# Kernel tuning notes

Hardware: AMD Instinct MI355X
Metric: run time of the kernel (lower is better)

The kernel has to match this reference:

```python
import jax, jax.numpy as jnp
import numpy as np

N_SRC_F = 40000; N_TGT_F = 40000; N_F = N_SRC_F + N_TGT_F
N_SRC_C = 1024; N_TGT_C = 1024; N_C = N_SRC_C + N_TGT_C
NN = 30        # KPConv neighbors per point
K = 15         # kernel points
C1 = 128       # fine-level feats (first_feats_dim)
C2 = 256       # coarse encoder out dim
GNN = 256      # gnn_feats_dim
HEADS = 4
DGCNN_K = 10
FINAL = 32     # final_feats_dim
EXT_F = 1.0; EXT_C = 2.0   # KPConv influence extents (scaled to unit-cube clouds)
EPS = 1e-12


def kpconv(q_pts, s_pts, s_feats, neighb, kpts, W, extent):
    # q_pts [Nq,3], s_pts [Ns,3], s_feats [Ns,Cin], neighb [Nq,NN], kpts [K,3], W [K,Cin,Cout]
    npts = s_pts[neighb]                              # [Nq,NN,3] irregular gather
    rel = npts - q_pts[:, None, :]
    # ||rel - kp||^2 expanded to avoid a [Nq,NN,K,3] intermediate
    d2 = (jnp.sum(rel * rel, -1)[:, :, None] + jnp.sum(kpts * kpts, -1)[None, None, :]
          - 2.0 * jnp.einsum('njd,kd->njk', rel, kpts))
    infl = jax.nn.relu(1.0 - jnp.sqrt(jnp.maximum(d2, EPS)) / extent)   # [Nq,NN,K]
    nf = s_feats[neighb]                              # [Nq,NN,Cin]
    h = jnp.einsum('njk,njc->nkc', infl, nf)          # kernel-point aggregation
    return jnp.einsum('nkc,kcd->nd', h, W)


def knn_idx(coords, k):
    sq = jnp.sum(coords * coords, -1)
    d2 = sq[:, None] + sq[None, :] - 2.0 * (coords @ coords.T)
    return jax.lax.top_k(-d2, k)[1]


def self_layer(coords, x, W, b):
    # DGCNN edge conv: knn on coords, edge = [x_i, x_j - x_i], 1x1 conv + relu, max over k
    idx = knn_idx(coords, DGCNN_K)
    neigh = x[idx]                                    # [N,k,C]
    ctr = jnp.broadcast_to(x[:, None, :], neigh.shape)
    edge = jnp.concatenate([ctr, neigh - ctr], -1)    # [N,k,2C]
    return jnp.max(jax.nn.relu(edge @ W + b), axis=1)


def cross_layer(x, y, Wq, Wk, Wv, Wm, bm):
    # multi-head cross attention x <- y, residual MLP on [x, message]
    N, C = x.shape
    dh = C // HEADS
    q = (x @ Wq).reshape(N, HEADS, dh)
    k = (y @ Wk).reshape(-1, HEADS, dh)
    v = (y @ Wv).reshape(-1, HEADS, dh)
    attn = jax.nn.softmax(jnp.einsum('nhd,mhd->hnm', q, k) / float(np.sqrt(dh)), axis=-1)
    msg = jnp.einsum('hnm,mhd->nhd', attn, v).reshape(N, C)
    return x + jnp.concatenate([x, msg], -1) @ Wm + bm


def l2norm(x):
    return x / jnp.maximum(jnp.linalg.norm(x, axis=1, keepdims=True), EPS)


def _forward(points_f, points_c, features, kernel_points_f, kernel_points_c,
             W_kp1, W_kp2, W_bottle, b_bottle, W_self1, b_self1,
             Wq, Wk, Wv, W_cross, b_cross, W_self2, b_self2,
             W_proj, b_proj, W_score, b_score, epsilon, W_dec, b_dec,
             neighbors_f, pool_idx, upsample_idx, len_src_c):
    # --- encoder: fine KPConv + strided KPConv to coarse ---
    x_f = kpconv(points_f, points_f, features, neighbors_f, kernel_points_f, W_kp1, EXT_F)  # [N_f,C1]
    skip = x_f
    x_c = kpconv(points_c, points_f, x_f, pool_idx, kernel_points_c, W_kp2, EXT_C)          # [N_c,C2]
    feats_c = x_c @ W_bottle + b_bottle                # bottleneck 1x1 conv -> [N_c,GNN]
    src, tgt = feats_c[:len_src_c], feats_c[len_src_c:]
    sc, tc = points_c[:len_src_c], points_c[len_src_c:]
    # --- GCN: self -> cross -> self (weights shared across src/tgt) ---
    src = self_layer(sc, src, W_self1, b_self1)
    tgt = self_layer(tc, tgt, W_self1, b_self1)
    src2 = cross_layer(src, tgt, Wq, Wk, Wv, W_cross, b_cross)
    tgt2 = cross_layer(tgt, src, Wq, Wk, Wv, W_cross, b_cross)
    src = self_layer(sc, src2, W_self2, b_self2)
    tgt = self_layer(tc, tgt2, W_self2, b_self2)
    feats = jnp.concatenate([src, tgt], 0) @ W_proj + b_proj   # proj_gnn
    scores_c_raw = feats @ W_score + b_score                   # proj_score [N_c,1]
    feats_norm = l2norm(feats)
    # --- bidirectional temperature-softmax matching head ---
    ip = feats_norm[:len_src_c] @ feats_norm[len_src_c:].T     # [Ns,Nt]
    temperature = jnp.exp(epsilon) + 0.03
    s1 = jax.nn.softmax(ip / temperature, axis=1) @ scores_c_raw[len_src_c:]
    s2 = jax.nn.softmax(ip.T / temperature, axis=1) @ scores_c_raw[:len_src_c]
    scores_saliency = jnp.concatenate([s1, s2], 0)
    # condition=True, add_cross_overlap=True branch
    x = jnp.concatenate([scores_c_raw, scores_saliency, feats], 1)    # [N_c, GNN+2]
    # --- decoder: nearest upsample + skip concat + unary conv ---
    x = jnp.concatenate([x[upsample_idx], skip], 1)            # [N_f, GNN+2+C1]
    x = x @ W_dec + b_dec                                      # [N_f, FINAL+2]
    feats_f = l2norm(x[:, :FINAL])
    so = jnp.clip(jax.nn.sigmoid(x[:, FINAL]), 0.0, 1.0)
    ss = jnp.clip(jax.nn.sigmoid(x[:, FINAL + 1]), 0.0, 1.0)
    so = jnp.where(jnp.isnan(so) | jnp.isinf(so), 0.0, so)     # regular_score
    ss = jnp.where(jnp.isnan(ss) | jnp.isinf(ss), 0.0, ss)
    return feats_f, so, ss


def _p(k, shape, fan):
    return jax.random.normal(k, shape, jnp.float32) / float(np.sqrt(fan))


def setup_inputs() -> dict:
    key = jax.random.key(0)
    ks = jax.random.split(key, 24)
    inp = {}
    inp['points_f'] = jax.random.uniform(ks[0], (N_F, 3), jnp.float32)
    inp['points_c'] = jax.random.uniform(ks[1], (N_C, 3), jnp.float32)
    inp['features'] = jnp.ones((N_F, 1), jnp.float32)
    inp['kernel_points_f'] = jax.random.normal(ks[2], (K, 3), jnp.float32) * 0.3
    inp['kernel_points_c'] = jax.random.normal(ks[3], (K, 3), jnp.float32) * 0.6
    inp['W_kp1'] = _p(ks[4], (K, 1, C1), K)
    inp['W_kp2'] = _p(ks[5], (K, C1, C2), K * C1)
    inp['W_bottle'] = _p(ks[6], (C2, GNN), C2); inp['b_bottle'] = jnp.zeros((GNN,), jnp.float32)
    inp['W_self1'] = _p(ks[7], (2 * GNN, GNN), 2 * GNN); inp['b_self1'] = jnp.zeros((GNN,), jnp.float32)
    inp['Wq'] = _p(ks[8], (GNN, GNN), GNN)
    inp['Wk'] = _p(ks[9], (GNN, GNN), GNN)
    inp['Wv'] = _p(ks[10], (GNN, GNN), GNN)
    inp['W_cross'] = _p(ks[11], (2 * GNN, GNN), 2 * GNN); inp['b_cross'] = jnp.zeros((GNN,), jnp.float32)
    inp['W_self2'] = _p(ks[12], (2 * GNN, GNN), 2 * GNN); inp['b_self2'] = jnp.zeros((GNN,), jnp.float32)
    inp['W_proj'] = _p(ks[13], (GNN, GNN), GNN); inp['b_proj'] = jnp.zeros((GNN,), jnp.float32)
    inp['W_score'] = _p(ks[14], (GNN, 1), GNN); inp['b_score'] = jnp.zeros((1,), jnp.float32)
    inp['epsilon'] = jnp.array(-5.0, jnp.float32)
    inp['W_dec'] = _p(ks[15], (GNN + 2 + C1, FINAL + 2), GNN + 2 + C1); inp['b_dec'] = jnp.zeros((FINAL + 2,), jnp.float32)
    inp['neighbors_f'] = jax.random.randint(ks[16], (N_F, NN), 0, N_F)
    inp['pool_idx'] = jax.random.randint(ks[17], (N_C, NN), 0, N_F)
    inp['upsample_idx'] = jax.random.randint(ks[18], (N_F,), 0, N_C)
    inp['len_src_c'] = N_SRC_C
    inp['len_src_f'] = N_SRC_F
    return inp


def reference(points_f, points_c, features, kernel_points_f, kernel_points_c,
              W_kp1, W_kp2, W_bottle, b_bottle, W_self1, b_self1,
              Wq, Wk, Wv, W_cross, b_cross, W_self2, b_self2,
              W_proj, b_proj, W_score, b_score, epsilon, W_dec, b_dec,
              neighbors_f, pool_idx, upsample_idx, len_src_c, len_src_f):
    return _forward(points_f, points_c, features, kernel_points_f, kernel_points_c,
                    W_kp1, W_kp2, W_bottle, b_bottle, W_self1, b_self1,
                    Wq, Wk, Wv, W_cross, b_cross, W_self2, b_self2,
                    W_proj, b_proj, W_score, b_score, epsilon, W_dec, b_dec,
                    neighbors_f, pool_idx, upsample_idx, len_src_c)
```

## Files before the change

### kernel.cpp

```cpp
#include <hip/hip_runtime.h>
#include <math.h>

#define NFINE   80000
#define NCRS    2048
#define NSRC    1024
#define NNB     30
#define KP      15
#define C1D     128
#define C2D     256
#define GD      256
#define DGK     10
#define FINALD  32
#define DECIN   386
#define DECOUT  34

#define NCHUNK  8
#define CHUNK   128
#define TK      32

__global__ __launch_bounds__(256) void kpconv_fine(
    const float* __restrict__ pts, const float* __restrict__ feat,
    const int* __restrict__ nbr, const float* __restrict__ kp,
    const float* __restrict__ W, float* __restrict__ out)
{
    int t = threadIdx.x, w = t >> 6, lane = t & 63;
    int n = blockIdx.x * 4 + w;
    __shared__ float contrib[4][NNB][17];
    __shared__ float h[4][KP + 1];
    float kx[KP], ky[KP], kz[KP], kk[KP];
#pragma unroll
    for (int k = 0; k < KP; k++) {
        kx[k] = kp[k*3]; ky[k] = kp[k*3+1]; kz[k] = kp[k*3+2];
        kk[k] = kx[k]*kx[k] + ky[k]*ky[k] + kz[k]*kz[k];
    }
    if (lane < NNB) {
        float qx = pts[n*3], qy = pts[n*3+1], qz = pts[n*3+2];
        int id = nbr[n*NNB + lane];
        float rx = pts[id*3]-qx, ry = pts[id*3+1]-qy, rz = pts[id*3+2]-qz;
        float rr = rx*rx + ry*ry + rz*rz;
        float f = feat[id];
#pragma unroll
        for (int k = 0; k < KP; k++) {
            float d2 = rr + kk[k] - 2.f*(rx*kx[k] + ry*ky[k] + rz*kz[k]);
            float infl = fmaxf(1.f - sqrtf(fmaxf(d2, 1e-12f)), 0.f);
            contrib[w][lane][k] = infl * f;
        }
    }
    __syncthreads();
    if (lane < KP) {
        float s = 0.f;
#pragma unroll
        for (int j = 0; j < NNB; j++) s += contrib[w][j][lane];
        h[w][lane] = s;
    }
    __syncthreads();
    float a0 = 0.f, a1 = 0.f;
#pragma unroll
    for (int k = 0; k < KP; k++) {
        float hk = h[w][k];
        a0 += hk * W[k*C1D + lane];
        a1 += hk * W[k*C1D + 64 + lane];
    }
    out[(size_t)n*C1D + lane]      = a0;
    out[(size_t)n*C1D + 64 + lane] = a1;
}

__global__ __launch_bounds__(256) void hh_kernel(
    const float* __restrict__ pc, const float* __restrict__ pf,
    const float* __restrict__ xf, const int* __restrict__ pool,
    const float* __restrict__ kp, float* __restrict__ hhg)
{
    int n = blockIdx.x, t = threadIdx.x;
    __shared__ float kx[KP], ky[KP], kz[KP], kk[KP];
    __shared__ float rel[NNB][4];
    __shared__ int   ids[NNB];
    __shared__ float infl[NNB][KP + 1];
    __shared__ float nf[NNB][C1D];
    if (t < KP) {
        float a = kp[t*3], b = kp[t*3+1], c = kp[t*3+2];
        kx[t] = a; ky[t] = b; kz[t] = c; kk[t] = a*a + b*b + c*c;
    }
    if (t < NNB) {
        int id = pool[n*NNB + t]; ids[t] = id;
        float qx = pc[n*3], qy = pc[n*3+1], qz = pc[n*3+2];
        float rx = pf[id*3]-qx, ry = pf[id*3+1]-qy, rz = pf[id*3+2]-qz;
        rel[t][0] = rx; rel[t][1] = ry; rel[t][2] = rz;
        rel[t][3] = rx*rx + ry*ry + rz*rz;
    }
    __syncthreads();
    for (int i = t; i < NNB*KP; i += 256) {
        int j = i / KP, kq = i % KP;
        float d2 = rel[j][3] + kk[kq]
                 - 2.f*(rel[j][0]*kx[kq] + rel[j][1]*ky[kq] + rel[j][2]*kz[kq]);
        infl[j][kq] = fmaxf(1.f - sqrtf(fmaxf(d2, 1e-12f)) * 0.5f, 0.f);
    }
    for (int i = t; i < NNB*C1D; i += 256) {
        int j = i >> 7, c = i & 127;
        nf[j][c] = xf[(size_t)ids[j]*C1D + c];
    }
    __syncthreads();
    for (int i = t; i < KP*C1D; i += 256) {
        int kq = i >> 7, c = i & 127;
        float s = 0.f;
#pragma unroll
        for (int j = 0; j < NNB; j++) s += infl[j][kq] * nf[j][c];
        hhg[(size_t)n*(KP*C1D) + i] = s;
    }
}

template<int CIN, int COUT, int TR, bool BIAS>
__global__ __launch_bounds__(COUT) void linear_rows(
    const float* __restrict__ in, const float* __restrict__ W,
    const float* __restrict__ b, float* __restrict__ out)
{
    int t = threadIdx.x, n0 = blockIdx.x * TR;
    __shared__ float xi[CIN][TR];
    for (int i = t; i < TR*CIN; i += COUT) {
        int r = i / CIN, c = i % CIN;
        xi[c][r] = in[(size_t)(n0+r)*CIN + c];
    }
    __syncthreads();
    float a[TR];
#pragma unroll
    for (int r = 0; r < TR; r++) a[r] = BIAS ? b[t] : 0.f;
    for (int c = 0; c < CIN; c++) {
        float wv = W[(size_t)c*COUT + t];
        float4 x0 = *(const float4*)&xi[c][0];
        a[0] += x0.x*wv; a[1] += x0.y*wv; a[2] += x0.z*wv; a[3] += x0.w*wv;
    }
#pragma unroll
    for (int r = 0; r < TR; r++) out[(size_t)(n0+r)*COUT + t] = a[r];
}

__global__ __launch_bounds__(512) void self_gemm(
    const float* __restrict__ x, const float* __restrict__ W,
    float* __restrict__ Y)
{
    int t = threadIdx.x, n0 = blockIdx.x * 4;
    __shared__ float xi[GD][4];
    for (int i = t; i < 4*GD; i += 512) {
        int r = i >> 8, c = i & 255;
        xi[c][r] = x[(size_t)(n0+r)*GD + c];
    }
    __syncthreads();
    const float* wcol = (t < GD) ? (W + t) : (W + (size_t)GD*GD + (t - GD));
    float a0 = 0.f, a1 = 0.f, a2 = 0.f, a3 = 0.f;
    for (int c = 0; c < GD; c++) {
        float wv = wcol[(size_t)c*GD];
        float4 xv = *(const float4*)&xi[c][0];
        a0 += xv.x*wv; a1 += xv.y*wv; a2 += xv.z*wv; a3 += xv.w*wv;
    }
    Y[(size_t)(n0+0)*512 + t] = a0;
    Y[(size_t)(n0+1)*512 + t] = a1;
    Y[(size_t)(n0+2)*512 + t] = a2;
    Y[(size_t)(n0+3)*512 + t] = a3;
}

__global__ __launch_bounds__(256) void edge_max(
    const float* __restrict__ Y, const int* __restrict__ knn,
    const float* __restrict__ b, float* __restrict__ out)
{
    int n = blockIdx.x, t = threadIdx.x;
    int base = (n < NSRC) ? 0 : NSRC;
    __shared__ int ids[DGK];
    if (t < DGK) ids[t] = base + knn[n*DGK + t];
    __syncthreads();
    float a  = Y[(size_t)n*512 + t];
    float bn = Y[(size_t)n*512 + GD + t];
    float cst = a - bn + b[t];
    float acc = 0.f;
#pragma unroll
    for (int j = 0; j < DGK; j++) {
        float bj = Y[(size_t)ids[j]*512 + GD + t];
        acc = fmaxf(acc, fmaxf(cst + bj, 0.f));
    }
    out[(size_t)n*GD + t] = acc;
}

__global__ __launch_bounds__(256) void qkv_kernel(
    const float* __restrict__ x, const float* __restrict__ Wq,
    const float* __restrict__ Wk, const float* __restrict__ Wv,
    float* __restrict__ qb, float* __restrict__ kb, float* __restrict__ vb)
{
    int t = threadIdx.x, n0 = blockIdx.x * 4;
    __shared__ float xi[GD][4];
    for (int i = t; i < 4*GD; i += 256) {
        int r = i >> 8, c = i & 255;
        xi[c][r] = x[(size_t)(n0+r)*GD + c];
    }
    __syncthreads();
    const float* Ws[3] = {Wq, Wk, Wv};
    float* outs[3] = {qb, kb, vb};
#pragma unroll
    for (int m = 0; m < 3; m++) {
        const float* W = Ws[m];
        float a0 = 0.f, a1 = 0.f, a2 = 0.f, a3 = 0.f;
        for (int c = 0; c < GD; c++) {
            float wv = W[c*GD + t];
            float4 xv = *(const float4*)&xi[c][0];
            a0 += xv.x*wv; a1 += xv.y*wv; a2 += xv.z*wv; a3 += xv.w*wv;
        }
        float* o = outs[m];
        o[(size_t)(n0+0)*GD + t] = a0;
        o[(size_t)(n0+1)*GD + t] = a1;
        o[(size_t)(n0+2)*GD + t] = a2;
        o[(size_t)(n0+3)*GD + t] = a3;
    }
}

__global__ __launch_bounds__(256) void knn_kernel(
    const float* __restrict__ pts, int* __restrict__ knn)
{
    int g = blockIdx.x;
    int t = threadIdx.x;
    int base = (g < NSRC) ? 0 : NSRC;
    int local = g - base;
    const float* P = pts + (size_t)base*3;
    __shared__ float d2s[NSRC];
    __shared__ float wval[4];
    __shared__ int   widx[4];
    float qx = P[local*3], qy = P[local*3+1], qz = P[local*3+2];
    float sqn = qx*qx + qy*qy + qz*qz;
#pragma unroll
    for (int ii = 0; ii < 4; ii++) {
        int m = t + ii*256;
        float px = P[m*3], py = P[m*3+1], pz = P[m*3+2];
        float sqm = px*px + py*py + pz*pz;
        d2s[m] = sqn + sqm - 2.f*(qx*px + qy*py + qz*pz);
    }
    __syncthreads();
    for (int r = 0; r < DGK; r++) {
        float bv = 3.4e38f; int bidx = NSRC;
#pragma unroll
        for (int ii = 0; ii < 4; ii++) {
            int m = t + ii*256;
            float v = d2s[m];
            if (v < bv) { bv = v; bidx = m; }
        }
#pragma unroll
        for (int off = 32; off >= 1; off >>= 1) {
            float ov = __shfl_xor(bv, off);
            int   oi = __shfl_xor(bidx, off);
            if (ov < bv || (ov == bv && oi < bidx)) { bv = ov; bidx = oi; }
        }
        if ((t & 63) == 0) { wval[t >> 6] = bv; widx[t >> 6] = bidx; }
        __syncthreads();
        if (t == 0) {
            float fv = wval[0]; int fi = widx[0];
#pragma unroll
            for (int wv2 = 1; wv2 < 4; wv2++)
                if (wval[wv2] < fv || (wval[wv2] == fv && widx[wv2] < fi)) {
                    fv = wval[wv2]; fi = widx[wv2];
                }
            knn[g*DGK + r] = fi;
            d2s[fi] = 3.4e38f;
        }
        __syncthreads();
    }
}

__global__ __launch_bounds__(256) void attn_flash(
    const float* __restrict__ qb, const float* __restrict__ kb,
    const float* __restrict__ vb, float* __restrict__ pm,
    float* __restrict__ pl, float* __restrict__ pacc)
{
    int bidx = blockIdx.x;
    int h = bidx & 3, chunk = (bidx >> 2) & 7, rb = bidx >> 5;
    int t = threadIdx.x;
    int u = t >> 2, li = t & 3;
    int row = rb * 64 + u;
    int kbase = (row < NSRC) ? NSRC : 0;

    __shared__ float4 kt[2][TK][16];
    __shared__ float4 vt[2][TK][16];

    const float4* kb4 = (const float4*)kb;
    const float4* vb4 = (const float4*)vb;
    size_t gbase = ((size_t)(kbase + chunk*CHUNK)) * 64 + h*16;

    float4 q[4];
    const float4* q4 = (const float4*)(qb + (size_t)row*GD + h*64 + li*16);
#pragma unroll
    for (int i = 0; i < 4; i++) q[i] = q4[i];
    float4 a[4];
#pragma unroll
    for (int i = 0; i < 4; i++) a[i] = make_float4(0.f, 0.f, 0.f, 0.f);
    float mr = -INFINITY, lr = 0.f;

    int f0 = t, f1 = t + 256;
    float4 rk0, rk1, rv0, rv1;

    {
        size_t tb = gbase;
        rk0 = kb4[tb + (size_t)(f0>>4)*64 + (f0&15)];
        rk1 = kb4[tb + (size_t)(f1>>4)*64 + (f1&15)];
        rv0 = vb4[tb + (size_t)(f0>>4)*64 + (f0&15)];
        rv1 = vb4[tb + (size_t)(f1>>4)*64 + (f1&15)];
        kt[0][f0>>4][f0&15] = rk0;  kt[0][f1>>4][f1&15] = rk1;
        vt[0][f0>>4][f0&15] = rv0;  vt[0][f1>>4][f1&15] = rv1;
    }
    __syncthreads();

    const int NT = CHUNK / TK;
    for (int tile = 0; tile < NT; tile++) {
        int cur = tile & 1;
        if (tile + 1 < NT) {
            size_t tb = gbase + (size_t)(tile+1)*TK*64;
            rk0 = kb4[tb + (size_t)(f0>>4)*64 + (f0&15)];
            rk1 = kb4[tb + (size_t)(f1>>4)*64 + (f1&15)];
            rv0 = vb4[tb + (size_t)(f0>>4)*64 + (f0&15)];
            rv1 = vb4[tb + (size_t)(f1>>4)*64 + (f1&15)];
        }
#pragma unroll 4
        for (int j = 0; j < TK; j++) {
            float4 k0 = kt[cur][j][li*4+0];
            float4 k1 = kt[cur][j][li*4+1];
            float4 k2 = kt[cur][j][li*4+2];
            float4 k3 = kt[cur][j][li*4+3];
            float d0 = q[0].x*k0.x + q[0].y*k0.y + q[0].z*k0.z + q[0].w*k0.w;
            float d1 = q[1].x*k1.x + q[1].y*k1.y + q[1].z*k1.z + q[1].w*k1.w;
            float d2 = q[2].x*k2.x + q[2].y*k2.y + q[2].z*k2.z + q[2].w*k2.w;
            float d3 = q[3].x*k3.x + q[3].y*k3.y + q[3].z*k3.z + q[3].w*k3.w;
            float p = (d0 + d1) + (d2 + d3);
            p += __shfl_xor(p, 1);
            p += __shfl_xor(p, 2);
            p *= 0.125f;
            float mn = fmaxf(mr, p);
            float sc = __expf(mr - mn);
            float e  = __expf(p - mn);
            lr = lr*sc + e;
            float4 v0 = vt[cur][j][li*4+0];
            float4 v1 = vt[cur][j][li*4+1];
            float4 v2 = vt[cur][j][li*4+2];
            float4 v3 = vt[cur][j][li*4+3];
            a[0].x = a[0].x*sc + e*v0.x; a[0].y = a[0].y*sc + e*v0.y;
            a[0].z = a[0].z*sc + e*v0.z; a[0].w = a[0].w*sc + e*v0.w;
            a[1].x = a[1].x*sc + e*v1.x; a[1].y = a[1].y*sc + e*v1.y;
            a[1].z = a[1].z*sc + e*v1.z; a[1].w = a[1].w*sc + e*v1.w;
            a[2].x = a[2].x*sc + e*v2.x; a[2].y = a[2].y*sc + e*v2.y;
            a[2].z = a[2].z*sc + e*v2.z; a[2].w = a[2].w*sc + e*v2.w;
            a[3].x = a[3].x*sc + e*v3.x; a[3].y = a[3].y*sc + e*v3.y;
            a[3].z = a[3].z*sc + e*v3.z; a[3].w = a[3].w*sc + e*v3.w;
            mr = mn;
        }
        if (tile + 1 < NT) {
            __syncthreads();
            int nb = (tile + 1) & 1;
            kt[nb][f0>>4][f0&15] = rk0;  kt[nb][f1>>4][f1&15] = rk1;
            vt[nb][f0>>4][f0&15] = rv0;  vt[nb][f1>>4][f1&15] = rv1;
            __syncthreads();
        }
    }
    int pi = (chunk*4 + h)*NCRS + row;
    if (li == 0) { pm[pi] = mr; pl[pi] = lr; }
    float4* po = (float4*)(pacc + (size_t)pi*64);
#pragma unroll
    for (int i = 0; i < 4; i++) po[li*4 + i] = a[i];
}

__global__ __launch_bounds__(256) void attn_combine(
    const float* __restrict__ pm, const float* __restrict__ pl,
    const float* __restrict__ pacc, float* __restrict__ msg)
{
    int row = blockIdx.x, t = threadIdx.x;
    int h = t >> 6, d = t & 63;
    float m = -INFINITY;
#pragma unroll
    for (int c = 0; c < NCHUNK; c++) m = fmaxf(m, pm[(c*4 + h)*NCRS + row]);
    float lsum = 0.f, asum = 0.f;
#pragma unroll
    for (int c = 0; c < NCHUNK; c++) {
        int pi = (c*4 + h)*NCRS + row;
        float w = __expf(pm[pi] - m);
        lsum += pl[pi] * w;
        asum += pacc[(size_t)pi*64 + d] * w;
    }
    msg[(size_t)row*GD + h*64 + d] = asum / lsum;
}

__global__ __launch_bounds__(256) void cross_combine(
    const float* __restrict__ x, const float* __restrict__ msg,
    const float* __restrict__ Wm, const float* __restrict__ bm,
    float* __restrict__ out)
{
    int t = threadIdx.x, n0 = blockIdx.x * 4;
    __shared__ float xs[GD][4], ms[GD][4];
    for (int i = t; i < 4*GD; i += 256) {
        int r = i >> 8, c = i & 255;
        xs[c][r] = x[(size_t)(n0+r)*GD + c];
        ms[c][r] = msg[(size_t)(n0+r)*GD + c];
    }
    __syncthreads();
    float a0 = bm[t], a1 = a0, a2 = a0, a3 = a0;
    for (int c = 0; c < GD; c++) {
        float w1 = Wm[c*GD + t];
        float w2 = Wm[(GD + c)*GD + t];
        float4 xv = *(const float4*)&xs[c][0];
        float4 mv = *(const float4*)&ms[c][0];
        a0 += xv.x*w1 + mv.x*w2; a1 += xv.y*w1 + mv.y*w2;
        a2 += xv.z*w1 + mv.z*w2; a3 += xv.w*w1 + mv.w*w2;
    }
    out[(size_t)(n0+0)*GD + t] = xs[t][0] + a0;
    out[(size_t)(n0+1)*GD + t] = xs[t][1] + a1;
    out[(size_t)(n0+2)*GD + t] = xs[t][2] + a2;
    out[(size_t)(n0+3)*GD + t] = xs[t][3] + a3;
}

__global__ __launch_bounds__(256) void proj_fused(
    const float* __restrict__ g3, const float* __restrict__ Wp,
    const float* __restrict__ bp, const float* __restrict__ Wsc,
    const float* __restrict__ bsc, float* __restrict__ feats,
    float* __restrict__ fnorm, float* __restrict__ scores)
{
    int n = blockIdx.x, t = threadIdx.x;
    __shared__ float xi[GD];
    __shared__ float red[256];
    xi[t] = g3[(size_t)n*GD + t];
    __syncthreads();
    float acc = bp[t];
    for (int c = 0; c < GD; c++) acc += xi[c] * Wp[c*GD + t];
    feats[(size_t)n*GD + t] = acc;
    red[t] = acc * acc; __syncthreads();
    for (int s = 128; s > 0; s >>= 1) { if (t < s) red[t] += red[t+s]; __syncthreads(); }
    float nrm = fmaxf(sqrtf(red[0]), 1e-12f);
    __syncthreads();
    fnorm[(size_t)n*GD + t] = acc / nrm;
    red[t] = acc * Wsc[t]; __syncthreads();
    for (int s = 128; s > 0; s >>= 1) { if (t < s) red[t] += red[t+s]; __syncthreads(); }
    if (t == 0) scores[n] = red[0] + bsc[0];
}

__global__ __launch_bounds__(256) void ip_kernel(
    const float* __restrict__ fnorm, float* __restrict__ ip)
{
    int t = threadIdx.x;
    int n0 = (blockIdx.x >> 2) * 4;
    int m  = (blockIdx.x & 3) * 256 + t;
    __shared__ float xs[GD][4];
    for (int i = t; i < 4*GD; i += 256) {
        int r = i >> 8, c = i & 255;
        xs[c][r] = fnorm[(size_t)(n0+r)*GD + c];
    }
    __syncthreads();
    const float4* fr = (const float4*)(fnorm + (size_t)(NSRC + m)*GD);
    float a0 = 0.f, a1 = 0.f, a2 = 0.f, a3 = 0.f;
    for (int c4 = 0; c4 < GD/4; c4++) {
        float4 f = fr[c4];
        float4 xa = *(const float4*)&xs[c4*4+0][0];
        float4 xb = *(const float4*)&xs[c4*4+1][0];
        float4 xc = *(const float4*)&xs[c4*4+2][0];
        float4 xd = *(const float4*)&xs[c4*4+3][0];
        a0 += f.x*xa.x + f.y*xb.x + f.z*xc.x + f.w*xd.x;
        a1 += f.x*xa.y + f.y*xb.y + f.z*xc.y + f.w*xd.y;
        a2 += f.x*xa.z + f.y*xb.z + f.z*xc.z + f.w*xd.z;
        a3 += f.x*xa.w + f.y*xb.w + f.z*xc.w + f.w*xd.w;
    }
    ip[(size_t)(n0+0)*NSRC + m] = a0;
    ip[(size_t)(n0+1)*NSRC + m] = a1;
    ip[(size_t)(n0+2)*NSRC + m] = a2;
    ip[(size_t)(n0+3)*NSRC + m] = a3;
}

template<bool COL>
__global__ __launch_bounds__(256) void saliency_kernel(
    const float* __restrict__ ip, const float* __restrict__ scores_other,
    const float* __restrict__ epsv, float* __restrict__ sal_out)
{
    int n = blockIdx.x, t = threadIdx.x;
    float T = expf(epsv[0]) + 0.03f;
    __shared__ float red[256];
    float vals[4];
    float m = -INFINITY;
#pragma unroll
    for (int ii = 0; ii < 4; ii++) {
        int i = t + ii*256;
        float vv = COL ? ip[(size_t)i*NSRC + n] : ip[(size_t)n*NSRC + i];
        vv /= T;
        vals[ii] = vv;
        m = fmaxf(m, vv);
    }
    red[t] = m; __syncthreads();
    for (int s = 128; s > 0; s >>= 1) { if (t < s) red[t] = fmaxf(red[t], red[t+s]); __syncthreads(); }
    float mx = red[0]; __syncthreads();
    float se = 0.f, wsum = 0.f;
#pragma unroll
    for (int ii = 0; ii < 4; ii++) {
        int i = t + ii*256;
        float e = expf(vals[ii] - mx);
        se += e; wsum += e * scores_other[i];
    }
    red[t] = se; __syncthreads();
    for (int s = 128; s > 0; s >>= 1) { if (t < s) red[t] += red[t+s]; __syncthreads(); }
    float S = red[0]; __syncthreads();
    red[t] = wsum; __syncthreads();
    for (int s = 128; s > 0; s >>= 1) { if (t < s) red[t] += red[t+s]; __syncthreads(); }
    if (t == 0) sal_out[n] = red[0] / S;
}

__global__ __launch_bounds__(256) void decoder_kernel(
    const float* __restrict__ feats, const float* __restrict__ scores,
    const float* __restrict__ sal, const float* __restrict__ skip,
    const int* __restrict__ ups, const float* __restrict__ Wd,
    const float* __restrict__ bd, float* __restrict__ outf,
    float* __restrict__ outso, float* __restrict__ outss)
{
    int row = blockIdx.x * 256 + threadIdx.x;
    if (row >= NFINE) return;
    int u = ups[row];
    float acc[DECOUT];
#pragma unroll
    for (int j = 0; j < DECOUT; j++) acc[j] = bd[j];
    float x0 = scores[u], x1 = sal[u];
#pragma unroll
    for (int j = 0; j < DECOUT; j++) acc[j] += x0 * Wd[j];
#pragma unroll
    for (int j = 0; j < DECOUT; j++) acc[j] += x1 * Wd[DECOUT + j];
    const float4* fr = (const float4*)(feats + (size_t)u * GD);
    for (int c4 = 0; c4 < GD/4; c4++) {
        float4 xv = fr[c4];
        const float* wr = Wd + (size_t)(2 + c4*4) * DECOUT;
#pragma unroll
        for (int j = 0; j < DECOUT; j++) acc[j] += xv.x * wr[j];
#pragma unroll
        for (int j = 0; j < DECOUT; j++) acc[j] += xv.y * wr[DECOUT + j];
#pragma unroll
        for (int j = 0; j < DECOUT; j++) acc[j] += xv.z * wr[2*DECOUT + j];
#pragma unroll
        for (int j = 0; j < DECOUT; j++) acc[j] += xv.w * wr[3*DECOUT + j];
    }
    const float4* sr = (const float4*)(skip + (size_t)row * C1D);
    for (int c4 = 0; c4 < C1D/4; c4++) {
        float4 xv = sr[c4];
        const float* wr = Wd + (size_t)(2 + GD + c4*4) * DECOUT;
#pragma unroll
        for (int j = 0; j < DECOUT; j++) acc[j] += xv.x * wr[j];
#pragma unroll
        for (int j = 0; j < DECOUT; j++) acc[j] += xv.y * wr[DECOUT + j];
#pragma unroll
        for (int j = 0; j < DECOUT; j++) acc[j] += xv.z * wr[2*DECOUT + j];
#pragma unroll
        for (int j = 0; j < DECOUT; j++) acc[j] += xv.w * wr[3*DECOUT + j];
    }
    float sq = 0.f;
#pragma unroll
    for (int j = 0; j < FINALD; j++) sq += acc[j]*acc[j];
    float inv = 1.f / fmaxf(sqrtf(sq), 1e-12f);
    float4* op = (float4*)(outf + (size_t)row * FINALD);
#pragma unroll
    for (int i = 0; i < 8; i++)
        op[i] = make_float4(acc[4*i]*inv, acc[4*i+1]*inv, acc[4*i+2]*inv, acc[4*i+3]*inv);
    float so = 1.f/(1.f + __expf(-acc[32]));
    so = fminf(fmaxf(so, 0.f), 1.f); if (!(so == so)) so = 0.f;
    float ss = 1.f/(1.f + __expf(-acc[33]));
    ss = fminf(fmaxf(ss, 0.f), 1.f); if (!(ss == ss)) ss = 0.f;
    outso[row] = so; outss[row] = ss;
}

extern "C" void kernel_launch(void* const* d_in, const int* in_sizes, int n_in,
                              void* d_out, int out_size, void* d_ws, size_t ws_size,
                              hipStream_t stream)
{
    const float* points_f     = (const float*)d_in[0];
    const float* points_c     = (const float*)d_in[1];
    const float* features     = (const float*)d_in[2];
    const float* kp_f         = (const float*)d_in[3];
    const float* kp_c         = (const float*)d_in[4];
    const float* W_kp1        = (const float*)d_in[5];
    const float* W_kp2        = (const float*)d_in[6];
    const float* W_bottle     = (const float*)d_in[7];
    const float* b_bottle     = (const float*)d_in[8];
    const float* W_self1      = (const float*)d_in[9];
    const float* b_self1      = (const float*)d_in[10];
    const float* Wq           = (const float*)d_in[11];
    const float* Wk           = (const float*)d_in[12];
    const float* Wv           = (const float*)d_in[13];
    const float* W_cross      = (const float*)d_in[14];
    const float* b_cross      = (const float*)d_in[15];
    const float* W_self2      = (const float*)d_in[16];
    const float* b_self2      = (const float*)d_in[17];
    const float* W_proj       = (const float*)d_in[18];
    const float* b_proj       = (const float*)d_in[19];
    const float* W_score      = (const float*)d_in[20];
    const float* b_score      = (const float*)d_in[21];
    const float* epsilon      = (const float*)d_in[22];
    const float* W_dec        = (const float*)d_in[23];
    const float* b_dec        = (const float*)d_in[24];
    const int*   neighbors_f  = (const int*)d_in[25];
    const int*   pool_idx     = (const int*)d_in[26];
    const int*   upsample_idx = (const int*)d_in[27];

    float* ws = (float*)d_ws;
    size_t o = 0;
    auto alloc = [&](size_t nfl) { float* p = ws + o; o += (nfl + 63) & ~(size_t)63; return p; };
    float* x_f     = alloc((size_t)NFINE * C1D);
    float* g1      = alloc((size_t)NCRS * GD);
    float* qb      = alloc((size_t)NCRS * GD);
    float* kb      = alloc((size_t)NCRS * GD);
    float* vb      = alloc((size_t)NCRS * GD);
    float* msg     = alloc((size_t)NCRS * GD);
    float* feats_c = alloc((size_t)NCRS * GD);
    float* scores  = alloc(NCRS);
    float* sal     = alloc(NCRS);
    int*   knn_b   = (int*)alloc(NCRS * DGK);

    const size_t NG = (size_t)NCRS * GD;
    size_t usz = (size_t)NCRS*C2D + (size_t)NCRS*KP*C1D;
    float* U = alloc(usz);
    float* x_c  = U;
    float* hhg  = U + (size_t)NCRS*C2D;
    float* Y1   = U;
    float* pm   = U;
    float* pl   = U + (size_t)NCRS*4*NCHUNK;
    float* pacc = U + (size_t)2*NCRS*4*NCHUNK;
    float* g2   = U;
    float* Y2   = U + NG;
    float* g3   = U + 3*NG;
    float* feats= U + 4*NG;
    float* fnorm= U + 5*NG;
    float* ip   = U + 6*NG;

    float* outf  = (float*)d_out;
    float* outso = outf + (size_t)NFINE * FINALD;
    float* outss = outso + NFINE;

    kpconv_fine<<<NFINE/4, 256, 0, stream>>>(points_f, features, neighbors_f, kp_f, W_kp1, x_f);
    hh_kernel<<<NCRS, 256, 0, stream>>>(points_c, points_f, x_f, pool_idx, kp_c, hhg);
    linear_rows<KP*C1D, C2D, 4, false><<<NCRS/4, C2D, 0, stream>>>(hhg, W_kp2, nullptr, x_c);
    linear_rows<C2D, GD, 4, true><<<NCRS/4, GD, 0, stream>>>(x_c, W_bottle, b_bottle, feats_c);

    knn_kernel<<<NCRS, 256, 0, stream>>>(points_c, knn_b);
    self_gemm<<<NCRS/4, 512, 0, stream>>>(feats_c, W_self1, Y1);
    edge_max<<<NCRS, 256, 0, stream>>>(Y1, knn_b, b_self1, g1);
    qkv_kernel<<<NCRS/4, 256, 0, stream>>>(g1, Wq, Wk, Wv, qb, kb, vb);
    attn_flash<<<1024, 256, 0, stream>>>(qb, kb, vb, pm, pl, pacc);
    attn_combine<<<NCRS, 256, 0, stream>>>(pm, pl, pacc, msg);
    cross_combine<<<NCRS/4, 256, 0, stream>>>(g1, msg, W_cross, b_cross, g2);
    self_gemm<<<NCRS/4, 512, 0, stream>>>(g2, W_self2, Y2);
    edge_max<<<NCRS, 256, 0, stream>>>(Y2, knn_b, b_self2, g3);

    proj_fused<<<NCRS, 256, 0, stream>>>(g3, W_proj, b_proj, W_score, b_score, feats, fnorm, scores);
    ip_kernel<<<NSRC, 256, 0, stream>>>(fnorm, ip);
    saliency_kernel<false><<<NSRC, 256, 0, stream>>>(ip, scores + NSRC, epsilon, sal);
    saliency_kernel<true><<<NSRC, 256, 0, stream>>>(ip, scores, epsilon, sal + NSRC);

    decoder_kernel<<<(NFINE + 255)/256, 256, 0, stream>>>(feats, scores, sal, x_f, upsample_idx,
                                                          W_dec, b_dec, outf, outso, outss);
}
```

Before: 493.0 us.

## Split-K kpconv GEMM, 8-row GEMM tiles, split proj/norm, precompute coarse decoder part

Replaces the KP*C1D→C2D linear with a split-K GEMM over 16-row tiles plus a fused reduction/bottleneck kernel, and widens all coarse GEMMs (self, qkv, cross, proj) to 8 rows per block with 4-way unrolled weight loads. The projection is split into a GEMM and a wave-shuffle norm/score kernel. The decoder's coarse contribution (feats, score, saliency) is computed once per coarse point and gathered per fine row, with skip weights staged in shared memory. This targets weight reload traffic and redundant per-fine-row coarse matmuls, at the cost of extra workspace and additional launches.

```diff
diff --git a/kernel.cpp b/kernel.cpp
--- a/kernel.cpp
+++ b/kernel.cpp
@@ -11,12 +11,14 @@
 #define GD      256
 #define DGK     10
 #define FINALD  32
-#define DECIN   386
 #define DECOUT  34
 
 #define NCHUNK  8
 #define CHUNK   128
 #define TK      32
+#define KC      4
+#define KSTEP   480
+#define GTR     16
 
 __global__ __launch_bounds__(256) void kpconv_fine(
     const float* __restrict__ pts, const float* __restrict__ feat,
@@ -108,52 +110,99 @@
     }
 }
 
-template<int CIN, int COUT, int TR, bool BIAS>
-__global__ __launch_bounds__(COUT) void linear_rows(
-    const float* __restrict__ in, const float* __restrict__ W,
+__global__ __launch_bounds__(256) void hh_gemm(
+    const float* __restrict__ hhg, const float* __restrict__ W,
+    float* __restrict__ pbuf)
+{
+    int t = threadIdx.x;
+    int rg = blockIdx.x >> 2, kc = blockIdx.x & 3;
+    int n0 = rg * GTR, kb0 = kc * KSTEP;
+    __shared__ float xi[GTR][KSTEP];
+    float* xf = &xi[0][0];
+    for (int i = t; i < GTR*KSTEP; i += 256) {
+        int r = i / KSTEP, c = i - r*KSTEP;
+        xf[i] = hhg[(size_t)(n0 + r)*(KP*C1D) + kb0 + c];
+    }
+    __syncthreads();
+    float a[GTR];
+#pragma unroll
+    for (int r = 0; r < GTR; r++) a[r] = 0.f;
+    for (int c = 0; c < KSTEP; c += 4) {
+        float w0 = W[(size_t)(kb0+c+0)*C2D + t];
+        float w1 = W[(size_t)(kb0+c+1)*C2D + t];
+        float w2 = W[(size_t)(kb0+c+2)*C2D + t];
+        float w3 = W[(size_t)(kb0+c+3)*C2D + t];
+#pragma unroll
+        for (int r = 0; r < GTR; r++) {
+            float4 xv = *(const float4*)&xi[r][c];
+            a[r] += xv.x*w0 + xv.y*w1 + xv.z*w2 + xv.w*w3;
+        }
+    }
+#pragma unroll
+    for (int r = 0; r < GTR; r++)
+        pbuf[(size_t)kc*NCRS*C2D + (size_t)(n0+r)*C2D + t] = a[r];
+}
+
+__global__ __launch_bounds__(256) void bottle_fused(
+    const float* __restrict__ pbuf, const float* __restrict__ Wb,
     const float* __restrict__ b, float* __restrict__ out)
 {
-    int t = threadIdx.x, n0 = blockIdx.x * TR;
-    __shared__ float xi[CIN][TR];
-    for (int i = t; i < TR*CIN; i += COUT) {
-        int r = i / CIN, c = i % CIN;
-        xi[c][r] = in[(size_t)(n0+r)*CIN + c];
-    }
-    __syncthreads();
-    float a[TR];
-#pragma unroll
-    for (int r = 0; r < TR; r++) a[r] = BIAS ? b[t] : 0.f;
-    for (int c = 0; c < CIN; c++) {
-        float wv = W[(size_t)c*COUT + t];
-        float4 x0 = *(const float4*)&xi[c][0];
-        a[0] += x0.x*wv; a[1] += x0.y*wv; a[2] += x0.z*wv; a[3] += x0.w*wv;
-    }
-#pragma unroll
-    for (int r = 0; r < TR; r++) out[(size_t)(n0+r)*COUT + t] = a[r];
+    int t = threadIdx.x, n0 = blockIdx.x * 8;
+    const size_t MN = (size_t)NCRS*C2D;
+    __shared__ float xi[8][C2D];
+    for (int i = t; i < 8*C2D; i += 256) {
+        int r = i >> 8, c = i & 255;
+        size_t off = (size_t)(n0+r)*C2D + c;
+        xi[r][c] = pbuf[off] + pbuf[MN+off] + pbuf[2*MN+off] + pbuf[3*MN+off];
+    }
+    __syncthreads();
+    float a[8];
+#pragma unroll
+    for (int r = 0; r < 8; r++) a[r] = 0.f;
+    for (int c = 0; c < C2D; c += 4) {
+        float w0 = Wb[(c+0)*GD + t];
+        float w1 = Wb[(c+1)*GD + t];
+        float w2 = Wb[(c+2)*GD + t];
+        float w3 = Wb[(c+3)*GD + t];
+#pragma unroll
+        for (int r = 0; r < 8; r++) {
+            float4 xv = *(const float4*)&xi[r][c];
+            a[r] += xv.x*w0 + xv.y*w1 + xv.z*w2 + xv.w*w3;
+        }
+    }
+    float bv = b[t];
+#pragma unroll
+    for (int r = 0; r < 8; r++) out[(size_t)(n0+r)*GD + t] = a[r] + bv;
 }
 
 __global__ __launch_bounds__(512) void self_gemm(
     const float* __restrict__ x, const float* __restrict__ W,
     float* __restrict__ Y)
 {
-    int t = threadIdx.x, n0 = blockIdx.x * 4;
-    __shared__ float xi[GD][4];
-    for (int i = t; i < 4*GD; i += 512) {
+    int t = threadIdx.x, n0 = blockIdx.x * 8;
+    __shared__ float xi[8][GD];
+    for (int i = t; i < 8*GD; i += 512) {
         int r = i >> 8, c = i & 255;
-        xi[c][r] = x[(size_t)(n0+r)*GD + c];
+        xi[r][c] = x[(size_t)(n0+r)*GD + c];
     }
     __syncthreads();
     const float* wcol = (t < GD) ? (W + t) : (W + (size_t)GD*GD + (t - GD));
-    float a0 = 0.f, a1 = 0.f, a2 = 0.f, a3 = 0.f;
-    for (int c = 0; c < GD; c++) {
-        float wv = wcol[(size_t)c*GD];
-        float4 xv = *(const float4*)&xi[c][0];
-        a0 += xv.x*wv; a1 += xv.y*wv; a2 += xv.z*wv; a3 += xv.w*wv;
-    }
-    Y[(size_t)(n0+0)*512 + t] = a0;
-    Y[(size_t)(n0+1)*512 + t] = a1;
-    Y[(size_t)(n0+2)*512 + t] = a2;
-    Y[(size_t)(n0+3)*512 + t] = a3;
+    float a[8];
+#pragma unroll
+    for (int r = 0; r < 8; r++) a[r] = 0.f;
+    for (int c = 0; c < GD; c += 4) {
+        float w0 = wcol[(size_t)(c+0)*GD];
+        float w1 = wcol[(size_t)(c+1)*GD];
+        float w2 = wcol[(size_t)(c+2)*GD];
+        float w3 = wcol[(size_t)(c+3)*GD];
+#pragma unroll
+        for (int r = 0; r < 8; r++) {
+            float4 xv = *(const float4*)&xi[r][c];
+            a[r] += xv.x*w0 + xv.y*w1 + xv.z*w2 + xv.w*w3;
+        }
+    }
+#pragma unroll
+    for (int r = 0; r < 8; r++) Y[(size_t)(n0+r)*512 + t] = a[r];
 }
 
 __global__ __launch_bounds__(256) void edge_max(
@@ -182,11 +231,11 @@
     const float* __restrict__ Wk, const float* __restrict__ Wv,
     float* __restrict__ qb, float* __restrict__ kb, float* __restrict__ vb)
 {
-    int t = threadIdx.x, n0 = blockIdx.x * 4;
-    __shared__ float xi[GD][4];
-    for (int i = t; i < 4*GD; i += 256) {
+    int t = threadIdx.x, n0 = blockIdx.x * 8;
+    __shared__ float xi[8][GD];
+    for (int i = t; i < 8*GD; i += 256) {
         int r = i >> 8, c = i & 255;
-        xi[c][r] = x[(size_t)(n0+r)*GD + c];
+        xi[r][c] = x[(size_t)(n0+r)*GD + c];
     }
     __syncthreads();
     const float* Ws[3] = {Wq, Wk, Wv};
@@ -194,17 +243,23 @@
 #pragma unroll
     for (int m = 0; m < 3; m++) {
         const float* W = Ws[m];
-        float a0 = 0.f, a1 = 0.f, a2 = 0.f, a3 = 0.f;
-        for (int c = 0; c < GD; c++) {
-            float wv = W[c*GD + t];
-            float4 xv = *(const float4*)&xi[c][0];
-            a0 += xv.x*wv; a1 += xv.y*wv; a2 += xv.z*wv; a3 += xv.w*wv;
+        float a[8];
+#pragma unroll
+        for (int r = 0; r < 8; r++) a[r] = 0.f;
+        for (int c = 0; c < GD; c += 4) {
+            float w0 = W[(c+0)*GD + t];
+            float w1 = W[(c+1)*GD + t];
+            float w2 = W[(c+2)*GD + t];
+            float w3 = W[(c+3)*GD + t];
+#pragma unroll
+            for (int r = 0; r < 8; r++) {
+                float4 xv = *(const float4*)&xi[r][c];
+                a[r] += xv.x*w0 + xv.y*w1 + xv.z*w2 + xv.w*w3;
+            }
         }
         float* o = outs[m];
-        o[(size_t)(n0+0)*GD + t] = a0;
-        o[(size_t)(n0+1)*GD + t] = a1;
-        o[(size_t)(n0+2)*GD + t] = a2;
-        o[(size_t)(n0+3)*GD + t] = a3;
+#pragma unroll
+        for (int r = 0; r < 8; r++) o[(size_t)(n0+r)*GD + t] = a[r];
     }
 }
 
@@ -383,51 +438,98 @@
     const float* __restrict__ Wm, const float* __restrict__ bm,
     float* __restrict__ out)
 {
-    int t = threadIdx.x, n0 = blockIdx.x * 4;
-    __shared__ float xs[GD][4], ms[GD][4];
-    for (int i = t; i < 4*GD; i += 256) {
+    int t = threadIdx.x, n0 = blockIdx.x * 8;
+    __shared__ float xs[8][GD], ms[8][GD];
+    for (int i = t; i < 8*GD; i += 256) {
         int r = i >> 8, c = i & 255;
-        xs[c][r] = x[(size_t)(n0+r)*GD + c];
-        ms[c][r] = msg[(size_t)(n0+r)*GD + c];
-    }
-    __syncthreads();
-    float a0 = bm[t], a1 = a0, a2 = a0, a3 = a0;
-    for (int c = 0; c < GD; c++) {
-        float w1 = Wm[c*GD + t];
-        float w2 = Wm[(GD + c)*GD + t];
-        float4 xv = *(const float4*)&xs[c][0];
-        float4 mv = *(const float4*)&ms[c][0];
-        a0 += xv.x*w1 + mv.x*w2; a1 += xv.y*w1 + mv.y*w2;
-        a2 += xv.z*w1 + mv.z*w2; a3 += xv.w*w1 + mv.w*w2;
-    }
-    out[(size_t)(n0+0)*GD + t] = xs[t][0] + a0;
-    out[(size_t)(n0+1)*GD + t] = xs[t][1] + a1;
-    out[(size_t)(n0+2)*GD + t] = xs[t][2] + a2;
-    out[(size_t)(n0+3)*GD + t] = xs[t][3] + a3;
-}
-
-__global__ __launch_bounds__(256) void proj_fused(
-    const float* __restrict__ g3, const float* __restrict__ Wp,
-    const float* __restrict__ bp, const float* __restrict__ Wsc,
-    const float* __restrict__ bsc, float* __restrict__ feats,
-    float* __restrict__ fnorm, float* __restrict__ scores)
-{
-    int n = blockIdx.x, t = threadIdx.x;
-    __shared__ float xi[GD];
-    __shared__ float red[256];
-    xi[t] = g3[(size_t)n*GD + t];
-    __syncthreads();
-    float acc = bp[t];
-    for (int c = 0; c < GD; c++) acc += xi[c] * Wp[c*GD + t];
-    feats[(size_t)n*GD + t] = acc;
-    red[t] = acc * acc; __syncthreads();
-    for (int s = 128; s > 0; s >>= 1) { if (t < s) red[t] += red[t+s]; __syncthreads(); }
-    float nrm = fmaxf(sqrtf(red[0]), 1e-12f);
-    __syncthreads();
-    fnorm[(size_t)n*GD + t] = acc / nrm;
-    red[t] = acc * Wsc[t]; __syncthreads();
-    for (int s = 128; s > 0; s >>= 1) { if (t < s) red[t] += red[t+s]; __syncthreads(); }
-    if (t == 0) scores[n] = red[0] + bsc[0];
+        xs[r][c] = x[(size_t)(n0+r)*GD + c];
+        ms[r][c] = msg[(size_t)(n0+r)*GD + c];
+    }
+    __syncthreads();
+    float bv = bm[t];
+    float a[8];
+#pragma unroll
+    for (int r = 0; r < 8; r++) a[r] = bv;
+    for (int c = 0; c < GD; c += 4) {
+        float w10 = Wm[(c+0)*GD + t];
+        float w11 = Wm[(c+1)*GD + t];
+        float w12 = Wm[(c+2)*GD + t];
+        float w13 = Wm[(c+3)*GD + t];
+        float w20 = Wm[(GD+c+0)*GD + t];
+        float w21 = Wm[(GD+c+1)*GD + t];
+        float w22 = Wm[(GD+c+2)*GD + t];
+        float w23 = Wm[(GD+c+3)*GD + t];
+#pragma unroll
+        for (int r = 0; r < 8; r++) {
+            float4 xv = *(const float4*)&xs[r][c];
+            float4 mv = *(const float4*)&ms[r][c];
+            a[r] += xv.x*w10 + xv.y*w11 + xv.z*w12 + xv.w*w13
+                  + mv.x*w20 + mv.y*w21 + mv.z*w22 + mv.w*w23;
+        }
+    }
+#pragma unroll
+    for (int r = 0; r < 8; r++)
+        out[(size_t)(n0+r)*GD + t] = xs[r][t] + a[r];
+}
+
+__global__ __launch_bounds__(256) void proj_gemm(
+    const float* __restrict__ x, const float* __restrict__ W,
+    const float* __restrict__ b, float* __restrict__ out)
+{
+    int t = threadIdx.x, n0 = blockIdx.x * 8;
+    __shared__ float xi[8][GD];
+    for (int i = t; i < 8*GD; i += 256) {
+        int r = i >> 8, c = i & 255;
+        xi[r][c] = x[(size_t)(n0+r)*GD + c];
+    }
+    __syncthreads();
+    float a[8];
+#pragma unroll
+    for (int r = 0; r < 8; r++) a[r] = 0.f;
+    for (int c = 0; c < GD; c += 4) {
+        float w0 = W[(c+0)*GD + t];
+        float w1 = W[(c+1)*GD + t];
+        float w2 = W[(c+2)*GD + t];
+        float w3 = W[(c+3)*GD + t];
+#pragma unroll
+        for (int r = 0; r < 8; r++) {
+            float4 xv = *(const float4*)&xi[r][c];
+            a[r] += xv.x*w0 + xv.y*w1 + xv.z*w2 + xv.w*w3;
+        }
+    }
+    float bv = b[t];
+#pragma unroll
+    for (int r = 0; r < 8; r++) out[(size_t)(n0+r)*GD + t] = a[r] + bv;
+}
+
+__global__ __launch_bounds__(256) void norm_score(
+    const float* __restrict__ feats, const float* __restrict__ Wsc,
+    const float* __restrict__ bsc, float* __restrict__ fnorm,
+    float* __restrict__ scores)
+{
+    int t = threadIdx.x, lane = t & 63, w = t >> 6;
+    int n0 = blockIdx.x * 8;
+#pragma unroll
+    for (int rr = 0; rr < 2; rr++) {
+        int r = n0 + w*2 + rr;
+        float q0 = feats[(size_t)r*GD + lane];
+        float q1 = feats[(size_t)r*GD + 64 + lane];
+        float q2 = feats[(size_t)r*GD + 128 + lane];
+        float q3 = feats[(size_t)r*GD + 192 + lane];
+        float sq = q0*q0 + q1*q1 + q2*q2 + q3*q3;
+        float sc = q0*Wsc[lane] + q1*Wsc[64+lane] + q2*Wsc[128+lane] + q3*Wsc[192+lane];
+#pragma unroll
+        for (int off = 32; off >= 1; off >>= 1) {
+            sq += __shfl_xor(sq, off);
+            sc += __shfl_xor(sc, off);
+        }
+        float inv = 1.f / fmaxf(sqrtf(sq), 1e-12f);
+        fnorm[(size_t)r*GD + lane]       = q0*inv;
+        fnorm[(size_t)r*GD + 64 + lane]  = q1*inv;
+        fnorm[(size_t)r*GD + 128 + lane] = q2*inv;
+        fnorm[(size_t)r*GD + 192 + lane] = q3*inv;
+        if (lane == 0) scores[r] = sc + bsc[0];
+    }
 }
 
 __global__ __launch_bounds__(256) void ip_kernel(
@@ -497,61 +599,71 @@
     if (t == 0) sal_out[n] = red[0] / S;
 }
 
+__global__ __launch_bounds__(256) void dec_coarse(
+    const float* __restrict__ scores, const float* __restrict__ sal,
+    const float* __restrict__ feats, const float* __restrict__ Wd,
+    const float* __restrict__ bd, float* __restrict__ decfeat)
+{
+    int t = threadIdx.x, lane = t & 63, w = t >> 6;
+    int n = blockIdx.x * 4 + w;
+    __shared__ float xr[4][GD];
+    for (int c = lane; c < GD; c += 64) xr[w][c] = feats[(size_t)n*GD + c];
+    float acc = 0.f;
+    if (lane < DECOUT) {
+        acc = bd[lane] + scores[n]*Wd[lane] + sal[n]*Wd[DECOUT + lane];
+        for (int c = 0; c < GD; c++) acc += xr[w][c] * Wd[(2 + c)*DECOUT + lane];
+    }
+    if (lane < 40) decfeat[(size_t)n*40 + lane] = (lane < DECOUT) ? acc : 0.f;
+}
+
 __global__ __launch_bounds__(256) void decoder_kernel(
-    const float* __restrict__ feats, const float* __restrict__ scores,
-    const float* __restrict__ sal, const float* __restrict__ skip,
+    const float* __restrict__ decfeat, const float* __restrict__ skip,
     const int* __restrict__ ups, const float* __restrict__ Wd,
-    const float* __restrict__ bd, float* __restrict__ outf,
-    float* __restrict__ outso, float* __restrict__ outss)
-{
-    int row = blockIdx.x * 256 + threadIdx.x;
+    float* __restrict__ outf, float* __restrict__ outso,
+    float* __restrict__ outss)
+{
+    int t = threadIdx.x;
+    __shared__ float wsk[C1D*36];
+    for (int i = t; i < C1D*36; i += 256) {
+        int cc = i / 36, j = i - cc*36;
+        wsk[i] = (j < DECOUT) ? Wd[(size_t)(2 + GD + cc)*DECOUT + j] : 0.f;
+    }
+    __syncthreads();
+    int row = blockIdx.x * 256 + t;
     if (row >= NFINE) return;
     int u = ups[row];
-    float acc[DECOUT];
-#pragma unroll
-    for (int j = 0; j < DECOUT; j++) acc[j] = bd[j];
-    float x0 = scores[u], x1 = sal[u];
-#pragma unroll
-    for (int j = 0; j < DECOUT; j++) acc[j] += x0 * Wd[j];
-#pragma unroll
-    for (int j = 0; j < DECOUT; j++) acc[j] += x1 * Wd[DECOUT + j];
-    const float4* fr = (const float4*)(feats + (size_t)u * GD);
-    for (int c4 = 0; c4 < GD/4; c4++) {
-        float4 xv = fr[c4];
-        const float* wr = Wd + (size_t)(2 + c4*4) * DECOUT;
-#pragma unroll
-        for (int j = 0; j < DECOUT; j++) acc[j] += xv.x * wr[j];
-#pragma unroll
-        for (int j = 0; j < DECOUT; j++) acc[j] += xv.y * wr[DECOUT + j];
-#pragma unroll
-        for (int j = 0; j < DECOUT; j++) acc[j] += xv.z * wr[2*DECOUT + j];
-#pragma unroll
-        for (int j = 0; j < DECOUT; j++) acc[j] += xv.w * wr[3*DECOUT + j];
-    }
-    const float4* sr = (const float4*)(skip + (size_t)row * C1D);
+    float4 acc[9];
+    const float4* df = (const float4*)(decfeat + (size_t)u*40);
+#pragma unroll
+    for (int q = 0; q < 9; q++) acc[q] = df[q];
+    const float4* sr = (const float4*)(skip + (size_t)row*C1D);
     for (int c4 = 0; c4 < C1D/4; c4++) {
         float4 xv = sr[c4];
-        const float* wr = Wd + (size_t)(2 + GD + c4*4) * DECOUT;
-#pragma unroll
-        for (int j = 0; j < DECOUT; j++) acc[j] += xv.x * wr[j];
-#pragma unroll
-        for (int j = 0; j < DECOUT; j++) acc[j] += xv.y * wr[DECOUT + j];
-#pragma unroll
-        for (int j = 0; j < DECOUT; j++) acc[j] += xv.z * wr[2*DECOUT + j];
-#pragma unroll
-        for (int j = 0; j < DECOUT; j++) acc[j] += xv.w * wr[3*DECOUT + j];
+        const float* wb = wsk + c4*4*36;
+#pragma unroll
+        for (int q = 0; q < 9; q++) {
+            float4 w0 = *(const float4*)&wb[q*4];
+            float4 w1 = *(const float4*)&wb[36 + q*4];
+            float4 w2 = *(const float4*)&wb[72 + q*4];
+            float4 w3 = *(const float4*)&wb[108 + q*4];
+            acc[q].x += xv.x*w0.x + xv.y*w1.x + xv.z*w2.x + xv.w*w3.x;
+            acc[q].y += xv.x*w0.y + xv.y*w1.y + xv.z*w2.y + xv.w*w3.y;
+            acc[q].z += xv.x*w0.z + xv.y*w1.z + xv.z*w2.z + xv.w*w3.z;
+            acc[q].w += xv.x*w0.w + xv.y*w1.w + xv.z*w2.w + xv.w*w3.w;
+        }
     }
     float sq = 0.f;
 #pragma unroll
-    for (int j = 0; j < FINALD; j++) sq += acc[j]*acc[j];
+    for (int q = 0; q < 8; q++)
+        sq += acc[q].x*acc[q].x + acc[q].y*acc[q].y + acc[q].z*acc[q].z + acc[q].w*acc[q].w;
     float inv = 1.f / fmaxf(sqrtf(sq), 1e-12f);
-    float4* op = (float4*)(outf + (size_t)row * FINALD);
-#pragma unroll
-    for (int i = 0; i < 8; i++)
-        op[i] = make_float4(acc[4*i]*inv, acc[4*i+1]*inv, acc[4*i+2]*inv, acc[4*i+3]*inv);
-    float so = 1.f/(1.f + __expf(-acc[32]));
+    float4* op = (float4*)(outf + (size_t)row*FINALD);
+#pragma unroll
+    for (int q = 0; q < 8; q++)
+        op[q] = make_float4(acc[q].x*inv, acc[q].y*inv, acc[q].z*inv, acc[q].w*inv);
+    float so = 1.f/(1.f + __expf(-acc[8].x));
     so = fminf(fmaxf(so, 0.f), 1.f); if (!(so == so)) so = 0.f;
-    float ss = 1.f/(1.f + __expf(-acc[33]));
+    float ss = 1.f/(1.f + __expf(-acc[8].y));
     ss = fminf(fmaxf(ss, 0.f), 1.f); if (!(ss == ss)) ss = 0.f;
     outso[row] = so; outss[row] = ss;
 }
@@ -601,13 +713,15 @@
     float* feats_c = alloc((size_t)NCRS * GD);
     float* scores  = alloc(NCRS);
     float* sal     = alloc(NCRS);
+    float* decfeat = alloc((size_t)NCRS * 40);
     int*   knn_b   = (int*)alloc(NCRS * DGK);
 
     const size_t NG = (size_t)NCRS * GD;
-    size_t usz = (size_t)NCRS*C2D + (size_t)NCRS*KP*C1D;
+    const size_t MN = (size_t)NCRS * C2D;
+    size_t usz = 4*MN + (size_t)NCRS*KP*C1D;
     float* U = alloc(usz);
-    float* x_c  = U;
-    float* hhg  = U + (size_t)NCRS*C2D;
+    float* pbuf = U;
+    float* hhg  = U + 4*MN;
     float* Y1   = U;
     float* pm   = U;
     float* pl   = U + (size_t)NCRS*4*NCHUNK;
@@ -625,24 +739,26 @@
 
     kpconv_fine<<<NFINE/4, 256, 0, stream>>>(points_f, features, neighbors_f, kp_f, W_kp1, x_f);
     hh_kernel<<<NCRS, 256, 0, stream>>>(points_c, points_f, x_f, pool_idx, kp_c, hhg);
-    linear_rows<KP*C1D, C2D, 4, false><<<NCRS/4, C2D, 0, stream>>>(hhg, W_kp2, nullptr, x_c);
-    linear_rows<C2D, GD, 4, true><<<NCRS/4, GD, 0, stream>>>(x_c, W_bottle, b_bottle, feats_c);
+    hh_gemm<<<(NCRS/GTR)*KC, 256, 0, stream>>>(hhg, W_kp2, pbuf);
+    bottle_fused<<<NCRS/8, 256, 0, stream>>>(pbuf, W_bottle, b_bottle, feats_c);
 
     knn_kernel<<<NCRS, 256, 0, stream>>>(points_c, knn_b);
-    self_gemm<<<NCRS/4, 512, 0, stream>>>(feats_c, W_self1, Y1);
+    self_gemm<<<NCRS/8, 512, 0, stream>>>(feats_c, W_self1, Y1);
     edge_max<<<NCRS, 256, 0, stream>>>(Y1, knn_b, b_self1, g1);
-    qkv_kernel<<<NCRS/4, 256, 0, stream>>>(g1, Wq, Wk, Wv, qb, kb, vb);
+    qkv_kernel<<<NCRS/8, 256, 0, stream>>>(g1, Wq, Wk, Wv, qb, kb, vb);
     attn_flash<<<1024, 256, 0, stream>>>(qb, kb, vb, pm, pl, pacc);
     attn_combine<<<NCRS, 256, 0, stream>>>(pm, pl, pacc, msg);
-    cross_combine<<<NCRS/4, 256, 0, stream>>>(g1, msg, W_cross, b_cross, g2);
-    self_gemm<<<NCRS/4, 512, 0, stream>>>(g2, W_self2, Y2);
+    cross_combine<<<NCRS/8, 256, 0, stream>>>(g1, msg, W_cross, b_cross, g2);
+    self_gemm<<<NCRS/8, 512, 0, stream>>>(g2, W_self2, Y2);
     edge_max<<<NCRS, 256, 0, stream>>>(Y2, knn_b, b_self2, g3);
 
-    proj_fused<<<NCRS, 256, 0, stream>>>(g3, W_proj, b_proj, W_score, b_score, feats, fnorm, scores);
+    proj_gemm<<<NCRS/8, 256, 0, stream>>>(g3, W_proj, b_proj, feats);
+    norm_score<<<NCRS/8, 256, 0, stream>>>(feats, W_score, b_score, fnorm, scores);
     ip_kernel<<<NSRC, 256, 0, stream>>>(fnorm, ip);
     saliency_kernel<false><<<NSRC, 256, 0, stream>>>(ip, scores + NSRC, epsilon, sal);
     saliency_kernel<true><<<NSRC, 256, 0, stream>>>(ip, scores, epsilon, sal + NSRC);
 
-    decoder_kernel<<<(NFINE + 255)/256, 256, 0, stream>>>(feats, scores, sal, x_f, upsample_idx,
-                                                          W_dec, b_dec, outf, outso, outss);
-}
+    dec_coarse<<<NCRS/4, 256, 0, stream>>>(scores, sal, feats, W_dec, b_dec, decfeat);
+    decoder_kernel<<<(NFINE + 255)/256, 256, 0, stream>>>(decfeat, x_f, upsample_idx,
+                                                          W_dec, outf, outso, outss);
+}
```

After: 500.7 us. About the same (+1.6%).
